# Kernel optimization log

Hardware: AMD Instinct MI355X
Metric: run time of the kernel (lower is better)

Reference implementation:

```python
import jax, jax.numpy as jnp
import numpy as np

B, C, N, F = 16, 12, 2048, 64

def setup_inputs() -> dict:
    key = jax.random.key(0)
    ks = jax.random.split(key, 6)
    x = jax.random.normal(ks[0], (B, C, N, F), dtype=jnp.float32)
    w1 = jax.random.normal(ks[1], (C,), dtype=jnp.float32) * (1.0 / np.sqrt(C))
    w2 = jax.random.normal(ks[2], (C, F), dtype=jnp.float32) * (1.0 / np.sqrt(F))
    w3 = jax.random.uniform(ks[3], (F,), dtype=jnp.float32)
    vs = jax.random.normal(ks[4], (N, N), dtype=jnp.float32) * (1.0 / np.sqrt(N))
    bs = jax.random.normal(ks[5], (N, N), dtype=jnp.float32) * (1.0 / np.sqrt(N))
    return {"x": x, "w1": w1, "w2": w2, "w3": w3, "vs": vs, "bs": bs}

def reference(x, w1, w2, w3, vs, bs):
    # w1: 1x1 conv over time dim -> contract c; then Linear(f_in, c_in) with weight (c, f)
    y1 = jnp.einsum('bcnf,c->bnf', x, w1)          # (B, N, F)
    y1 = jnp.einsum('bnf,cf->bnc', y1, w2)         # (B, N, C)
    y2 = jnp.einsum('bcnf,f->bcn', x, w3)          # (B, C, N)
    product = jnp.einsum('bnc,bcm->bnm', y1, y2)   # (B, N, N)
    s = jax.nn.sigmoid(product + bs)               # (B, N, N)
    y = jnp.einsum('nm,bmk->bnk', vs, s)           # (B, N, N)
    return jax.nn.softmax(y, axis=-1)
```

## Files before the change

### kernel.cpp

```cpp
#include <hip/hip_runtime.h>
#include <hip/hip_bf16.h>

#define BB 16
#define CC 12
#define NN 2048
#define FF 64

typedef __bf16 bf16;
typedef __bf16 bf16x8 __attribute__((ext_vector_type(8)));
typedef float  f32x4  __attribute__((ext_vector_type(4)));

#define AS1(p) ((__attribute__((address_space(1))) void*)(p))
#define AS3(p) ((__attribute__((address_space(3))) void*)(p))

__global__ __launch_bounds__(256) void k_prep_vs(const float* __restrict__ vs,
                                                 bf16* __restrict__ vsb) {
    int n = blockIdx.x;
    int t = threadIdx.x;
    int m = t * 8;
    const float4* src = (const float4*)(vs + (size_t)n * NN + m);
    float4 a = src[0], b = src[1];
    bf16x8 v;
    v[0] = (bf16)a.x; v[1] = (bf16)a.y; v[2] = (bf16)a.z; v[3] = (bf16)a.w;
    v[4] = (bf16)b.x; v[5] = (bf16)b.y; v[6] = (bf16)b.z; v[7] = (bf16)b.w;
    int msw = m ^ ((n & 7) << 3);
    *(bf16x8*)(vsb + (size_t)n * NN + msw) = v;
}

__global__ __launch_bounds__(256) void k_front(const float* __restrict__ x,
                                               const float* __restrict__ w1,
                                               const float* __restrict__ w2,
                                               const float* __restrict__ w3,
                                               float* __restrict__ y1b,
                                               float* __restrict__ y2) {
    int b  = blockIdx.x >> 5;
    int n0 = (blockIdx.x & 31) * 64;
    int t  = threadIdx.x;
    int nl = t >> 2;
    int fq = t & 3;

    float w3v[4][4];
#pragma unroll
    for (int ii = 0; ii < 4; ii++) {
        float4 w = *(const float4*)(w3 + ii * 16 + fq * 4);
        w3v[ii][0] = w.x; w3v[ii][1] = w.y; w3v[ii][2] = w.z; w3v[ii][3] = w.w;
    }

    float acc[4][4];
#pragma unroll
    for (int ii = 0; ii < 4; ii++)
#pragma unroll
        for (int j = 0; j < 4; j++) acc[ii][j] = 0.f;

    const size_t bstride = (size_t)CC * NN * FF;
    for (int c = 0; c < CC; c++) {
        float w1c = w1[c];
        const float* xp = x + (size_t)b * bstride + (size_t)c * NN * FF
                            + (size_t)(n0 + nl) * FF;
        float p2 = 0.f;
#pragma unroll
        for (int ii = 0; ii < 4; ii++) {
            float4 v = *(const float4*)(xp + ii * 16 + fq * 4);
            acc[ii][0] += w1c * v.x; acc[ii][1] += w1c * v.y;
            acc[ii][2] += w1c * v.z; acc[ii][3] += w1c * v.w;
            p2 += v.x * w3v[ii][0] + v.y * w3v[ii][1]
                + v.z * w3v[ii][2] + v.w * w3v[ii][3];
        }
        p2 += __shfl_xor(p2, 1);
        p2 += __shfl_xor(p2, 2);
        if (fq == 0) y2[((size_t)b * CC + c) * NN + n0 + nl] = p2;
    }

#pragma unroll
    for (int c2 = 0; c2 < CC; c2++) {
        float p = 0.f;
#pragma unroll
        for (int ii = 0; ii < 4; ii++) {
            float4 w = *(const float4*)(w2 + c2 * FF + ii * 16 + fq * 4);
            p += acc[ii][0] * w.x + acc[ii][1] * w.y
               + acc[ii][2] * w.z + acc[ii][3] * w.w;
        }
        p += __shfl_xor(p, 1);
        p += __shfl_xor(p, 2);
        if (fq == 0) y1b[((size_t)b * NN + n0 + nl) * CC + c2] = p;
    }
}

__global__ __launch_bounds__(256) void k_score(const float* __restrict__ y1b,
                                               const float* __restrict__ y2,
                                               const float* __restrict__ bs,
                                               bf16* __restrict__ st) {
    int m0 = blockIdx.x * 64;
    int k0 = blockIdx.y * 64;
    int b  = blockIdx.z;
    int t  = threadIdx.x;

    __shared__ float bsl[64][65];
    __shared__ float y2l[12][64];

    {
        int r = t >> 2, cq = (t & 3) * 16;
        const float4* src = (const float4*)(bs + (size_t)(m0 + r) * NN + k0 + cq);
#pragma unroll
        for (int q = 0; q < 4; q++) {
            float4 v = src[q];
            bsl[r][cq + q * 4 + 0] = v.x;
            bsl[r][cq + q * 4 + 1] = v.y;
            bsl[r][cq + q * 4 + 2] = v.z;
            bsl[r][cq + q * 4 + 3] = v.w;
        }
    }
    if (t < 192) {
        int c = t >> 4, off = (t & 15) * 4;
        float4 v = *(const float4*)(y2 + ((size_t)b * CC + c) * NN + k0 + off);
        *(float4*)&y2l[c][off] = v;
    }

    int i = t & 63;
    const float* yp = y1b + ((size_t)b * NN + m0 + i) * CC;
    float4 a0 = *(const float4*)yp;
    float4 a1 = *(const float4*)(yp + 4);
    float4 a2 = *(const float4*)(yp + 8);
    float yv[12] = {a0.x,a0.y,a0.z,a0.w, a1.x,a1.y,a1.z,a1.w, a2.x,a2.y,a2.z,a2.w};

    __syncthreads();

    int jg = t >> 6;
    bf16* ob = st + (size_t)b * NN * NN;
#pragma unroll
    for (int jj = 0; jj < 16; jj++) {
        int j = jg * 16 + jj;
        int k = k0 + j;
        float p = bsl[i][j];
#pragma unroll
        for (int c = 0; c < CC; c++) p += yv[c] * y2l[c][j];
        float s = 1.f / (1.f + __expf(-p));
        int msw = i ^ ((k & 7) << 3);
        ob[(size_t)k * NN + m0 + msw] = (bf16)s;
    }
}

__global__ __launch_bounds__(256) void k_gemm(const bf16* __restrict__ vsb,
                                              const bf16* __restrict__ st,
                                              float* __restrict__ y) {
    __shared__ __align__(1024) char lds_raw[32768];
    char* ldsA = lds_raw;
    char* ldsB = lds_raw + 16384;

    int n0 = blockIdx.x * 128;
    int k0 = blockIdx.y * 128;
    int b  = blockIdx.z;
    int t  = threadIdx.x;
    int w  = t >> 6, l = t & 63;
    int wn = w >> 1, wk = w & 1;

    const bf16* gA = vsb + (size_t)n0 * NN;
    const bf16* gB = st + (size_t)b * NN * NN + (size_t)k0 * NN;

    int srow = l >> 3;
    int scol = (l & 7) * 8;

    f32x4 acc[4][4];
#pragma unroll
    for (int fi = 0; fi < 4; fi++)
#pragma unroll
        for (int fj = 0; fj < 4; fj++) acc[fi][fj] = (f32x4){0.f, 0.f, 0.f, 0.f};

    for (int mt = 0; mt < NN / 64; mt++) {
        __syncthreads();
        int mbase = mt * 64;
#pragma unroll
        for (int q = 0; q < 4; q++) {
            int ch  = w * 4 + q;
            int row = ch * 8 + srow;
            __builtin_amdgcn_global_load_lds(
                AS1(gA + (size_t)row * NN + mbase + scol),
                AS3(ldsA + ch * 1024), 16, 0, 0);
            __builtin_amdgcn_global_load_lds(
                AS1(gB + (size_t)row * NN + mbase + scol),
                AS3(ldsB + ch * 1024), 16, 0, 0);
        }
        __syncthreads();

#pragma unroll
        for (int ks = 0; ks < 2; ks++) {
            bf16x8 af[4], bfr[4];
            int ebyte = (ks * 32 + (l >> 4) * 8) * 2;
#pragma unroll
            for (int fi = 0; fi < 4; fi++) {
                int r = wn * 64 + fi * 16 + (l & 15);
                af[fi] = *(const bf16x8*)(ldsA + r * 128 + (ebyte ^ ((r & 7) << 4)));
            }
#pragma unroll
            for (int fj = 0; fj < 4; fj++) {
                int r = wk * 64 + fj * 16 + (l & 15);
                bfr[fj] = *(const bf16x8*)(ldsB + r * 128 + (ebyte ^ ((r & 7) << 4)));
            }
#pragma unroll
            for (int fi = 0; fi < 4; fi++)
#pragma unroll
                for (int fj = 0; fj < 4; fj++)
                    acc[fi][fj] = __builtin_amdgcn_mfma_f32_16x16x32_bf16(
                        af[fi], bfr[fj], acc[fi][fj], 0, 0, 0);
        }
    }

    float* yb = y + (size_t)b * NN * NN;
#pragma unroll
    for (int fi = 0; fi < 4; fi++) {
#pragma unroll
        for (int fj = 0; fj < 4; fj++) {
            int col = k0 + wk * 64 + fj * 16 + (l & 15);
#pragma unroll
            for (int rr = 0; rr < 4; rr++) {
                int row = n0 + wn * 64 + fi * 16 + (l >> 4) * 4 + rr;
                yb[(size_t)row * NN + col] = acc[fi][fj][rr];
            }
        }
    }
}

__global__ __launch_bounds__(256) void k_softmax(float* __restrict__ y) {
    int n = blockIdx.x, b = blockIdx.y;
    float* row = y + ((size_t)b * NN + n) * NN;
    int t = threadIdx.x;
    int l = t & 63, w = t >> 6;

    float4 v0 = *(const float4*)(row + t * 4);
    float4 v1 = *(const float4*)(row + 1024 + t * 4);

    float mx = fmaxf(fmaxf(fmaxf(v0.x, v0.y), fmaxf(v0.z, v0.w)),
                     fmaxf(fmaxf(v1.x, v1.y), fmaxf(v1.z, v1.w)));
#pragma unroll
    for (int s = 1; s < 64; s <<= 1) mx = fmaxf(mx, __shfl_xor(mx, s));

    __shared__ float redm[4];
    if (l == 0) redm[w] = mx;
    __syncthreads();
    mx = fmaxf(fmaxf(redm[0], redm[1]), fmaxf(redm[2], redm[3]));

    float e[8];
    e[0] = __expf(v0.x - mx); e[1] = __expf(v0.y - mx);
    e[2] = __expf(v0.z - mx); e[3] = __expf(v0.w - mx);
    e[4] = __expf(v1.x - mx); e[5] = __expf(v1.y - mx);
    e[6] = __expf(v1.z - mx); e[7] = __expf(v1.w - mx);
    float sum = ((e[0] + e[1]) + (e[2] + e[3])) + ((e[4] + e[5]) + (e[6] + e[7]));
#pragma unroll
    for (int s = 1; s < 64; s <<= 1) sum += __shfl_xor(sum, s);

    __shared__ float reds[4];
    if (l == 0) reds[w] = sum;
    __syncthreads();
    sum = (reds[0] + reds[1]) + (reds[2] + reds[3]);
    float inv = 1.f / sum;

    float4 o0 = {e[0] * inv, e[1] * inv, e[2] * inv, e[3] * inv};
    float4 o1 = {e[4] * inv, e[5] * inv, e[6] * inv, e[7] * inv};
    *(float4*)(row + t * 4) = o0;
    *(float4*)(row + 1024 + t * 4) = o1;
}

extern "C" void kernel_launch(void* const* d_in, const int* in_sizes, int n_in,
                              void* d_out, int out_size, void* d_ws, size_t ws_size,
                              hipStream_t stream) {
    (void)in_sizes; (void)n_in; (void)out_size; (void)ws_size;
    const float* x  = (const float*)d_in[0];
    const float* w1 = (const float*)d_in[1];
    const float* w2 = (const float*)d_in[2];
    const float* w3 = (const float*)d_in[3];
    const float* vs = (const float*)d_in[4];
    const float* bs = (const float*)d_in[5];
    float* out = (float*)d_out;

    char* ws = (char*)d_ws;
    bf16* st  = (bf16*)ws;
    bf16* vsb = (bf16*)(ws + (size_t)BB * NN * NN * 2);
    float* y1b = (float*)(ws + (size_t)BB * NN * NN * 2 + (size_t)NN * NN * 2);
    float* y2  = y1b + (size_t)BB * NN * CC;

    k_prep_vs<<<dim3(NN), 256, 0, stream>>>(vs, vsb);
    k_front<<<dim3(BB * (NN / 64)), 256, 0, stream>>>(x, w1, w2, w3, y1b, y2);
    k_score<<<dim3(NN / 64, NN / 64, BB), 256, 0, stream>>>(y1b, y2, bs, st);
    k_gemm<<<dim3(NN / 128, NN / 128, BB), 256, 0, stream>>>(vsb, st, out);
    k_softmax<<<dim3(NN, BB), 256, 0, stream>>>(out);
}
```

Baseline: 832.1 us.

## Rewrite batched GEMM with 256x256 tiles, double-buffered LDS prefetch and new swizzle

Replaces the 128x128 single-buffered GEMM with a 512-thread, 256x256-tile kernel. It double-buffers 64-wide K slices in 128KB of LDS and issues global-to-LDS loads two stages ahead, interleaved with MFMA groups. Barriers wait on vmcnt, and s_setprio raises priority around the MFMA bursts. The bf16 swizzle in the producer kernels changes to match the new LDS read pattern. The aims are to hide global load latency and to double operand reuse per tile, at the cost of heavy LDS and register use and fewer blocks for the GPU.

Measured after the change: 727.3 us. 1.14x faster.

```diff
diff --git a/kernel.cpp b/kernel.cpp
--- a/kernel.cpp
+++ b/kernel.cpp
@@ -12,6 +12,7 @@
 
 #define AS1(p) ((__attribute__((address_space(1))) void*)(p))
 #define AS3(p) ((__attribute__((address_space(3))) void*)(p))
+
 
 __global__ __launch_bounds__(256) void k_prep_vs(const float* __restrict__ vs,
                                                  bf16* __restrict__ vsb) {
@@ -23,7 +24,7 @@
     bf16x8 v;
     v[0] = (bf16)a.x; v[1] = (bf16)a.y; v[2] = (bf16)a.z; v[3] = (bf16)a.w;
     v[4] = (bf16)b.x; v[5] = (bf16)b.y; v[6] = (bf16)b.z; v[7] = (bf16)b.w;
-    int msw = m ^ ((n & 7) << 3);
+    int msw = m ^ (((n >> 1) & 3) << 3);
     *(bf16x8*)(vsb + (size_t)n * NN + msw) = v;
 }
 
@@ -135,89 +136,147 @@
 #pragma unroll
         for (int c = 0; c < CC; c++) p += yv[c] * y2l[c][j];
         float s = 1.f / (1.f + __expf(-p));
-        int msw = i ^ ((k & 7) << 3);
+        int msw = i ^ (((k >> 1) & 3) << 3);
         ob[(size_t)k * NN + m0 + msw] = (bf16)s;
     }
 }
 
-__global__ __launch_bounds__(256) void k_gemm(const bf16* __restrict__ vsb,
-                                              const bf16* __restrict__ st,
-                                              float* __restrict__ y) {
-    __shared__ __align__(1024) char lds_raw[32768];
-    char* ldsA = lds_raw;
-    char* ldsB = lds_raw + 16384;
-
-    int n0 = blockIdx.x * 128;
-    int k0 = blockIdx.y * 128;
-    int b  = blockIdx.z;
-    int t  = threadIdx.x;
-    int w  = t >> 6, l = t & 63;
-    int wn = w >> 1, wk = w & 1;
+__global__ __launch_bounds__(512, 2) void k_gemm(const bf16* __restrict__ vsb,
+                                                 const bf16* __restrict__ st,
+                                                 float* __restrict__ y) {
+    __shared__ __align__(1024) char lds[131072];
+
+    const int t  = threadIdx.x;
+    const int w  = t >> 6, l = t & 63;
+    const int wm = w >> 2, wn = w & 3;
+    const int n0 = blockIdx.x * 256, k0 = blockIdx.y * 256, b = blockIdx.z;
 
     const bf16* gA = vsb + (size_t)n0 * NN;
     const bf16* gB = st + (size_t)b * NN * NN + (size_t)k0 * NN;
 
-    int srow = l >> 3;
-    int scol = (l & 7) * 8;
-
-    f32x4 acc[4][4];
-#pragma unroll
-    for (int fi = 0; fi < 4; fi++)
+    const int rq = l >> 2;
+    const int cq = (l & 3) * 8;
+    const int g0 = w * 2;
+
+    const int pbase = (l & 15) * 64 + (((l >> 4) ^ ((l >> 1) & 3)) << 4);
+
+    auto stage = [&](const bf16* src, int ldsOff, int ks, int mt, int d) {
+#pragma unroll
+        for (int i = 0; i < 2; i++) {
+            int g = g0 + i;
+            __builtin_amdgcn_global_load_lds(
+                AS1(src + (size_t)(g * 16 + rq) * NN + mt * 64 + ks * 32 + cq),
+                AS3(lds + ldsOff + d * 32768 + (g * 2 + ks) * 1024), 16, 0, 0);
+        }
+    };
+
+    f32x4 acc[8][4];
+#pragma unroll
+    for (int fi = 0; fi < 8; fi++)
 #pragma unroll
         for (int fj = 0; fj < 4; fj++) acc[fi][fj] = (f32x4){0.f, 0.f, 0.f, 0.f};
 
-    for (int mt = 0; mt < NN / 64; mt++) {
-        __syncthreads();
-        int mbase = mt * 64;
-#pragma unroll
-        for (int q = 0; q < 4; q++) {
-            int ch  = w * 4 + q;
-            int row = ch * 8 + srow;
-            __builtin_amdgcn_global_load_lds(
-                AS1(gA + (size_t)row * NN + mbase + scol),
-                AS3(ldsA + ch * 1024), 16, 0, 0);
-            __builtin_amdgcn_global_load_lds(
-                AS1(gB + (size_t)row * NN + mbase + scol),
-                AS3(ldsB + ch * 1024), 16, 0, 0);
-        }
-        __syncthreads();
-
-#pragma unroll
-        for (int ks = 0; ks < 2; ks++) {
-            bf16x8 af[4], bfr[4];
-            int ebyte = (ks * 32 + (l >> 4) * 8) * 2;
-#pragma unroll
-            for (int fi = 0; fi < 4; fi++) {
-                int r = wn * 64 + fi * 16 + (l & 15);
-                af[fi] = *(const bf16x8*)(ldsA + r * 128 + (ebyte ^ ((r & 7) << 4)));
+    stage(gA, 0, 0, 0, 0);     stage(gB, 65536, 0, 0, 0);
+    stage(gA, 0, 1, 0, 0);     stage(gB, 65536, 1, 0, 0);
+    stage(gA, 0, 0, 1, 1);     stage(gB, 65536, 0, 1, 1);
+    asm volatile("s_waitcnt vmcnt(8)" ::: "memory");
+    __builtin_amdgcn_s_barrier();
+    asm volatile("" ::: "memory");
+
+    for (int kt = 0; kt < 32; kt++) {
+        const int d = kt & 1, dn = d ^ 1;
+        const int tn1 = (kt + 1 < 32) ? kt + 1 : 31;
+        const int tn2 = (kt + 2 < 32) ? kt + 2 : 31;
+        const char* Ab = lds + d * 32768 + wm * 16384;
+        const char* Bb = lds + 65536 + d * 32768 + wn * 8192;
+
+        bf16x8 aq[4], bq[4];
+
+        stage(gA, 0, 1, tn1, dn);
+#pragma unroll
+        for (int fj = 0; fj < 4; fj++)
+            bq[fj] = *(const bf16x8*)(Bb + fj * 2048 + pbase);
+#pragma unroll
+        for (int fi = 0; fi < 4; fi++)
+            aq[fi] = *(const bf16x8*)(Ab + fi * 2048 + pbase);
+        __builtin_amdgcn_s_setprio(1);
+#pragma unroll
+        for (int fi = 0; fi < 4; fi++)
+#pragma unroll
+            for (int fj = 0; fj < 4; fj++)
+                acc[fi][fj] = __builtin_amdgcn_mfma_f32_16x16x32_bf16(
+                    aq[fi], bq[fj], acc[fi][fj], 0, 0, 0);
+        __builtin_amdgcn_s_setprio(0);
+
+        stage(gB, 65536, 1, tn1, dn);
+#pragma unroll
+        for (int fi = 0; fi < 4; fi++)
+            aq[fi] = *(const bf16x8*)(Ab + 8192 + fi * 2048 + pbase);
+        __builtin_amdgcn_s_setprio(1);
+#pragma unroll
+        for (int fi = 0; fi < 4; fi++)
+#pragma unroll
+            for (int fj = 0; fj < 4; fj++)
+                acc[4 + fi][fj] = __builtin_amdgcn_mfma_f32_16x16x32_bf16(
+                    aq[fi], bq[fj], acc[4 + fi][fj], 0, 0, 0);
+        __builtin_amdgcn_s_setprio(0);
+
+        asm volatile("s_waitcnt lgkmcnt(0)" ::: "memory");
+        asm volatile("s_waitcnt vmcnt(8)" ::: "memory");
+        __builtin_amdgcn_s_barrier();
+        asm volatile("" ::: "memory");
+
+        stage(gA, 0, 0, tn2, d);
+#pragma unroll
+        for (int fj = 0; fj < 4; fj++)
+            bq[fj] = *(const bf16x8*)(Bb + 1024 + fj * 2048 + pbase);
+#pragma unroll
+        for (int fi = 0; fi < 4; fi++)
+            aq[fi] = *(const bf16x8*)(Ab + 1024 + fi * 2048 + pbase);
+        __builtin_amdgcn_s_setprio(1);
+#pragma unroll
+        for (int fi = 0; fi < 4; fi++)
+#pragma unroll
+            for (int fj = 0; fj < 4; fj++)
+                acc[fi][fj] = __builtin_amdgcn_mfma_f32_16x16x32_bf16(
+                    aq[fi], bq[fj], acc[fi][fj], 0, 0, 0);
+        __builtin_amdgcn_s_setprio(0);
+
+        stage(gB, 65536, 0, tn2, d);
+#pragma unroll
+        for (int fi = 0; fi < 4; fi++)
+            aq[fi] = *(const bf16x8*)(Ab + 8192 + 1024 + fi * 2048 + pbase);
+        __builtin_amdgcn_s_setprio(1);
+#pragma unroll
+        for (int fi = 0; fi < 4; fi++)
+#pragma unroll
+            for (int fj = 0; fj < 4; fj++)
+                acc[4 + fi][fj] = __builtin_amdgcn_mfma_f32_16x16x32_bf16(
+                    aq[fi], bq[fj], acc[4 + fi][fj], 0, 0, 0);
+        __builtin_amdgcn_s_setprio(0);
+
+        asm volatile("s_waitcnt lgkmcnt(0)" ::: "memory");
+        asm volatile("s_waitcnt vmcnt(8)" ::: "memory");
+        __builtin_amdgcn_s_barrier();
+        asm volatile("" ::: "memory");
+    }
+
+    asm volatile("s_waitcnt vmcnt(0)" ::: "memory");
+
+    float* yb = y + (size_t)b * NN * NN;
+#pragma unroll
+    for (int rh = 0; rh < 2; rh++)
+#pragma unroll
+        for (int fi = 0; fi < 4; fi++)
+#pragma unroll
+            for (int fj = 0; fj < 4; fj++) {
+                int col = k0 + wn * 64 + fj * 16 + (l & 15);
+#pragma unroll
+                for (int rr = 0; rr < 4; rr++) {
+                    int row = n0 + wm * 128 + rh * 64 + fi * 16 + (l >> 4) * 4 + rr;
+                    yb[(size_t)row * NN + col] = acc[rh * 4 + fi][fj][rr];
+                }
             }
-#pragma unroll
-            for (int fj = 0; fj < 4; fj++) {
-                int r = wk * 64 + fj * 16 + (l & 15);
-                bfr[fj] = *(const bf16x8*)(ldsB + r * 128 + (ebyte ^ ((r & 7) << 4)));
-            }
-#pragma unroll
-            for (int fi = 0; fi < 4; fi++)
-#pragma unroll
-                for (int fj = 0; fj < 4; fj++)
-                    acc[fi][fj] = __builtin_amdgcn_mfma_f32_16x16x32_bf16(
-                        af[fi], bfr[fj], acc[fi][fj], 0, 0, 0);
-        }
-    }
-
-    float* yb = y + (size_t)b * NN * NN;
-#pragma unroll
-    for (int fi = 0; fi < 4; fi++) {
-#pragma unroll
-        for (int fj = 0; fj < 4; fj++) {
-            int col = k0 + wk * 64 + fj * 16 + (l & 15);
-#pragma unroll
-            for (int rr = 0; rr < 4; rr++) {
-                int row = n0 + wn * 64 + fi * 16 + (l >> 4) * 4 + rr;
-                yb[(size_t)row * NN + col] = acc[fi][fj][rr];
-            }
-        }
-    }
 }
 
 __global__ __launch_bounds__(256) void k_softmax(float* __restrict__ y) {
@@ -281,6 +340,6 @@
     k_prep_vs<<<dim3(NN), 256, 0, stream>>>(vs, vsb);
     k_front<<<dim3(BB * (NN / 64)), 256, 0, stream>>>(x, w1, w2, w3, y1b, y2);
     k_score<<<dim3(NN / 64, NN / 64, BB), 256, 0, stream>>>(y1b, y2, bs, st);
-    k_gemm<<<dim3(NN / 128, NN / 128, BB), 256, 0, stream>>>(vsb, st, out);
+    k_gemm<<<dim3(NN / 256, NN / 256, BB), 512, 0, stream>>>(vsb, st, out);
     k_softmax<<<dim3(NN, BB), 256, 0, stream>>>(out);
 }
```
